# Optimization experiments

Hardware: AMD Instinct MI355X
Metric: run time of the kernel (lower is better)

The kernel has to match this reference:

```python
import jax, jax.numpy as jnp
import numpy as np

T, B, OBS, LS, H, NA = 256, 1024, 128, 128, 128, 18


def setup_inputs() -> dict:
    key = jax.random.key(0)
    ks = jax.random.split(key, 20)
    rn = lambda i, shape, sc: jax.random.normal(ks[i], shape, dtype=jnp.float32) * sc
    return {
        "x": jax.random.normal(ks[0], (T * B, OBS), dtype=jnp.float32),
        "done": (jax.random.uniform(ks[1], (T * B,)) < 0.05).astype(jnp.float32),
        "h0": rn(2, (1, B, H), 0.1),
        "c0": rn(3, (1, B, H), 0.1),
        # MLP encoder: obs -> 128 -> 32 -> lstm_size
        "W1": rn(4, (128, OBS), 0.1), "b1": jnp.zeros((128,), jnp.float32),
        "W2": rn(5, (32, 128), 0.1), "b2": jnp.zeros((32,), jnp.float32),
        "W3": rn(6, (LS, 32), 0.1), "b3": jnp.zeros((LS,), jnp.float32),
        # LSTM params, PyTorch gate order [i, f, g, o]
        "Wih": rn(7, (4 * H, LS), 0.1), "Whh": rn(8, (4 * H, H), 0.1),
        "bih": jnp.zeros((4 * H,), jnp.float32), "bhh": jnp.zeros((4 * H,), jnp.float32),
        "Wa": rn(9, (NA, H), 0.01), "ba": jnp.zeros((NA,), jnp.float32),
        "Wc": rn(10, (1, H), 0.1), "bc": jnp.zeros((1,), jnp.float32),
    }


def reference(x, done, h0, c0, W1, b1, W2, b2, W3, b3, Wih, Whh, bih, bhh, Wa, ba, Wc, bc):
    # MLP encoder (self.network)
    hid = jax.nn.relu(x @ W1.T + b1)
    hid = jax.nn.relu(hid @ W2.T + b2)
    hid = jax.nn.relu(hid @ W3.T + b3)           # [T*B, LS]
    Bsz = h0.shape[1]
    hid = hid.reshape(-1, Bsz, hid.shape[-1])    # [T, B, LS]
    d = done.reshape(-1, Bsz)                    # [T, B]

    Hh = h0.shape[-1]

    def step(carry, inp):
        h, c = carry
        xt, dt = inp
        m = (1.0 - dt)[:, None]                  # reset mask
        h = h * m
        c = c * m
        gates = xt @ Wih.T + bih + h @ Whh.T + bhh   # [B, 4H]
        i = jax.nn.sigmoid(gates[:, :Hh])
        f = jax.nn.sigmoid(gates[:, Hh:2 * Hh])
        g = jnp.tanh(gates[:, 2 * Hh:3 * Hh])
        o = jax.nn.sigmoid(gates[:, 3 * Hh:])
        c = f * c + i * g
        h = o * jnp.tanh(c)
        return (h, c), h

    (hN, cN), hs = jax.lax.scan(step, (h0[0], c0[0]), (hid, d))
    flat = hs.reshape(-1, Hh)                    # [T*B, H]
    logits = flat @ Wa.T + ba                    # actor head
    value = flat @ Wc.T + bc                     # critic head
    return jnp.concatenate([logits, value], axis=-1)  # [T*B, NA+1]
```

## Files before the change

kernel.cpp:

```cpp
#include <hip/hip_runtime.h>
#include <hip/hip_bf16.h>

typedef unsigned short u16;
typedef unsigned int u32;
typedef __attribute__((ext_vector_type(8))) short short8;
typedef __attribute__((ext_vector_type(4))) float f4;
typedef __attribute__((ext_vector_type(4))) u32 u4;

#define MFMA(a, b, c) __builtin_amdgcn_mfma_f32_16x16x32_bf16((a), (b), (c), 0, 0, 0)

#define TT 256
#define BB 1024
#define NN (TT * BB)
#define L2E 1.442695040888963f
#define WS_HID3 0
#define WS_WF   (NN * 128)
#define OFF_W1  0
#define OFF_W2  16384
#define OFF_W3  20480
#define OFF_WIH 24576
#define OFF_WHH 90112
#define OFF_WA  155648
#define WF_TOT  159744

static __device__ __forceinline__ u16 f2bf(float f) {
    u32 u = __float_as_uint(f);
    u32 r = (u + 0x7FFFu + ((u >> 16) & 1u)) >> 16;
    return (u16)r;
}
static __device__ __forceinline__ short8 pack8(f4 a, f4 b) {
    short8 r;
    r[0] = (short)f2bf(a[0]); r[1] = (short)f2bf(a[1]);
    r[2] = (short)f2bf(a[2]); r[3] = (short)f2bf(a[3]);
    r[4] = (short)f2bf(b[0]); r[5] = (short)f2bf(b[1]);
    r[6] = (short)f2bf(b[2]); r[7] = (short)f2bf(b[3]);
    return r;
}
static __device__ __forceinline__ short8 u4_to_s8(u4 v) {
    union { u4 u; short8 s; } t; t.u = v; return t.s;
}
static __device__ __forceinline__ float sig_pre(float x) {
    return __builtin_amdgcn_rcpf(1.f + __builtin_amdgcn_exp2f(-x));
}
static __device__ __forceinline__ float tanhf_fast(float x) {
    return 2.f * __builtin_amdgcn_rcpf(1.f + __builtin_amdgcn_exp2f(-2.885390081777927f * x)) - 1.f;
}

static __device__ void convW128(const float* src, int Nn, u16* dst, int tid, int nth) {
    int tot = Nn * 128;
    for (int d = tid; d < tot; d += nth) {
        int j = d & 7, l = (d >> 3) & 63, ck = d >> 9;
        int kc = ck & 3, nt = ck >> 2;
        int n = nt * 16 + (l & 15), k = kc * 32 + ((l >> 4) << 3) + j;
        dst[d] = f2bf(src[n * 128 + k]);
    }
}
static __device__ void convW128g(const float* src, u16* dst, int tid, int nth) {
    int tot = 512 * 128;
    for (int d = tid; d < tot; d += nth) {
        int j = d & 7, l = (d >> 3) & 63, ck = d >> 9;
        int kc = ck & 3, nt = ck >> 2;
        int n = nt * 16 + (l & 15), k = kc * 32 + ((l >> 4) << 3) + j;
        float sc = ((n >> 7) == 2) ? (2.f * L2E) : L2E;
        dst[d] = f2bf(src[n * 128 + k] * sc);
    }
}
static __device__ void convW32(const float* src, int Nn, u16* dst, int tid, int nth) {
    int tot = Nn * 32;
    for (int d = tid; d < tot; d += nth) {
        int j = d & 7, l = (d >> 3) & 63, nt = d >> 9;
        int n = nt * 16 + (l & 15), k = ((l >> 4) << 3) + j;
        dst[d] = f2bf(src[n * 32 + k]);
    }
}

__global__ void k0_conv(const float* __restrict__ W1, const float* __restrict__ W2,
                        const float* __restrict__ W3, const float* __restrict__ Wih,
                        const float* __restrict__ Whh, const float* __restrict__ Wa,
                        const float* __restrict__ Wc, u16* __restrict__ wf) {
    int tid = blockIdx.x * blockDim.x + threadIdx.x;
    int nth = gridDim.x * blockDim.x;
    convW128(W1, 128, wf + OFF_W1, tid, nth);
    convW128(W2, 32, wf + OFF_W2, tid, nth);
    convW32(W3, 128, wf + OFF_W3, tid, nth);
    convW128g(Wih, wf + OFF_WIH, tid, nth);
    convW128g(Whh, wf + OFF_WHH, tid, nth);
    for (int d = tid; d < 32 * 128; d += nth) {
        int j = d & 7, l = (d >> 3) & 63, ck = d >> 9;
        int kc = ck & 3, nt = ck >> 2;
        int n = nt * 16 + (l & 15), k = kc * 32 + ((l >> 4) << 3) + j;
        float v = (n < 18) ? Wa[n * 128 + k] : ((n == 18) ? Wc[k] : 0.f);
        wf[OFF_WA + d] = f2bf(v);
    }
}

__global__ __launch_bounds__(256, 2) void k1_enc(
    const float* __restrict__ x, const float* __restrict__ b1, const float* __restrict__ b2,
    const float* __restrict__ b3, const u16* __restrict__ wf, u16* __restrict__ hid3f) {
    __shared__ __align__(16) u16 scr[4][2560];

    int tid = threadIdx.x, wv = tid >> 6, lane = tid & 63;
    int m = lane & 15, q = lane >> 4;
    u16* s1 = scr[wv];
    u16* s2 = scr[wv] + 2048;
    const short8* W1v = (const short8*)(wf + OFF_W1);
    const short8* W2v = (const short8*)(wf + OFF_W2);
    const short8* W3v = (const short8*)(wf + OFF_W3);
    short8 w1r[32], w3r[8];
#pragma unroll
    for (int i = 0; i < 32; ++i) w1r[i] = W1v[i * 64 + lane];
#pragma unroll
    for (int i = 0; i < 8; ++i) w3r[i] = W3v[i * 64 + lane];
    int wid = blockIdx.x * 4 + wv;

    for (int it = 0; it < 8; ++it) {
        int c = wid + it * 2048;
        short8 a1[4];
        const float* xr = x + (size_t)(c * 16 + m) * 128 + q * 8;
#pragma unroll
        for (int kc = 0; kc < 4; ++kc) {
            f4 f0 = *(const f4*)(xr + kc * 32);
            f4 f1 = *(const f4*)(xr + kc * 32 + 4);
            a1[kc] = pack8(f0, f1);
        }
#pragma unroll
        for (int nt = 0; nt < 8; ++nt) {
            f4 acc = {0.f, 0.f, 0.f, 0.f};
#pragma unroll
            for (int kc = 0; kc < 4; ++kc) acc = MFMA(a1[kc], w1r[nt * 4 + kc], acc);
            int col = nt * 16 + m;
            float bb = b1[col];
            int base = (col >> 5) * 512 + ((col >> 3) & 3) * 128 + (col & 7);
#pragma unroll
            for (int p = 0; p < 4; ++p) {
                float v = acc[p] + bb; v = v > 0.f ? v : 0.f;
                s1[base + (q * 4 + p) * 8] = f2bf(v);
            }
        }
        asm volatile("s_waitcnt lgkmcnt(0)" ::: "memory");
        short8 a2[4];
#pragma unroll
        for (int kc = 0; kc < 4; ++kc) a2[kc] = *(const short8*)(s1 + kc * 512 + lane * 8);
#pragma unroll
        for (int nt = 0; nt < 2; ++nt) {
            f4 acc = {0.f, 0.f, 0.f, 0.f};
#pragma unroll
            for (int kc = 0; kc < 4; ++kc) acc = MFMA(a2[kc], W2v[(nt * 4 + kc) * 64 + lane], acc);
            int col = nt * 16 + m;
            float bb = b2[col];
            int base = (col >> 3) * 128 + (col & 7);
#pragma unroll
            for (int p = 0; p < 4; ++p) {
                float v = acc[p] + bb; v = v > 0.f ? v : 0.f;
                s2[base + (q * 4 + p) * 8] = f2bf(v);
            }
        }
        asm volatile("s_waitcnt lgkmcnt(0)" ::: "memory");
        short8 a3 = *(const short8*)(s2 + lane * 8);
#pragma unroll
        for (int nt = 0; nt < 8; ++nt) {
            f4 acc = {0.f, 0.f, 0.f, 0.f};
            acc = MFMA(a3, w3r[nt], acc);
            int col = nt * 16 + m;
            float bb = b3[col];
            int base = (col >> 5) * 512 + ((col >> 3) & 3) * 128 + (col & 7);
#pragma unroll
            for (int p = 0; p < 4; ++p) {
                float v = acc[p] + bb; v = v > 0.f ? v : 0.f;
                s1[base + (q * 4 + p) * 8] = f2bf(v);
            }
        }
        asm volatile("s_waitcnt lgkmcnt(0)" ::: "memory");
        int bI = c & 63, tt = c >> 6;
        u4* dst = (u4*)hid3f + ((size_t)bI * 256 + tt) * 256;
#pragma unroll
        for (int kc = 0; kc < 4; ++kc) dst[kc * 64 + lane] = *(const u4*)(s1 + kc * 512 + lane * 8);
    }
}

__global__ __launch_bounds__(512, 1) void k3_scan(
    const u16* __restrict__ hid3, const u16* __restrict__ wf,
    const float* __restrict__ bih, const float* __restrict__ bhh,
    const float* __restrict__ done, const float* __restrict__ h0, const float* __restrict__ c0,
    const float* __restrict__ ba, const float* __restrict__ bc, float* __restrict__ out) {
    __shared__ __align__(16) u16 hbuf[2][2048];
    __shared__ __align__(16) float dls[4096];

    int tid = threadIdx.x, wv = tid >> 6, lane = tid & 63;
    int m = lane & 15, q = lane >> 4;
    int bI = blockIdx.x, rb = bI * 16;
    int u = wv * 16 + m;

    const short8* WHv = (const short8*)(wf + OFF_WHH);
    const short8* WIv = (const short8*)(wf + OFF_WIH);
    const short8* WAv = (const short8*)(wf + OFF_WA);
    short8 wh[4][4], wi[4][4];
#pragma unroll
    for (int g = 0; g < 4; ++g)
#pragma unroll
        for (int kc = 0; kc < 4; ++kc) {
            int nt = g * 8 + wv;
            wh[g][kc] = WHv[(nt * 4 + kc) * 64 + lane];
            wi[g][kc] = WIv[(nt * 4 + kc) * 64 + lane];
        }
    float bg[4];
#pragma unroll
    for (int g = 0; g < 4; ++g) {
        float sc = (g == 2) ? (2.f * L2E) : L2E;
        bg[g] = (bih[g * 128 + u] + bhh[g * 128 + u]) * sc;
    }
    short8 wab[4];
    float hb = 0.f;
    int hcol = wv * 16 + m;
    if (wv < 2) {
#pragma unroll
        for (int kc = 0; kc < 4; ++kc) wab[kc] = WAv[(wv * 4 + kc) * 64 + lane];
        if (hcol < 18) hb = ba[hcol];
        else if (hcol == 18) hb = bc[0];
    }

    for (int i = tid; i < 4096; i += 512) {
        int t = i >> 4, r = i & 15;
        dls[i] = 1.0f - done[(size_t)t * BB + rb + r];
    }
    float cst[4];
#pragma unroll
    for (int k = 0; k < 4; ++k) {
        int r = 4 * q + k;
        cst[k] = c0[(size_t)(rb + r) * 128 + u];
        float hv = h0[(size_t)(rb + r) * 128 + u];
        hbuf[0][(u >> 5) * 512 + (((u >> 3) & 3) * 16 + r) * 8 + (u & 7)] = f2bf(hv);
    }
    const u4* h3 = (const u4*)hid3 + (size_t)bI * 65536;
    u4 xf[4];
#pragma unroll
    for (int kc = 0; kc < 4; ++kc) xf[kc] = h3[kc * 64 + lane];
    __syncthreads();

    for (int t = 0; t < TT; ++t) {
        const u16* hc = hbuf[t & 1];
        u16* hn = hbuf[(t + 1) & 1];
        short8 ah[4];
#pragma unroll
        for (int kc = 0; kc < 4; ++kc) ah[kc] = *(const short8*)(hc + kc * 512 + lane * 8);
        f4 aH[4], aX[4];
#pragma unroll
        for (int g = 0; g < 4; ++g) {
            aH[g] = (f4){0.f, 0.f, 0.f, 0.f};
            aX[g] = (f4){bg[g], bg[g], bg[g], bg[g]};
        }
#pragma unroll
        for (int kc = 0; kc < 4; ++kc) {
            short8 xs = u4_to_s8(xf[kc]);
#pragma unroll
            for (int g = 0; g < 4; ++g) {
                aH[g] = MFMA(ah[kc], wh[g][kc], aH[g]);
                aX[g] = MFMA(xs, wi[g][kc], aX[g]);
            }
        }
        if (t < TT - 1) {
#pragma unroll
            for (int kc = 0; kc < 4; ++kc)
                xf[kc] = h3[(size_t)(t + 1) * 256 + kc * 64 + lane];
        }
        if (wv < 2 && t > 0) {
            f4 hacc = {0.f, 0.f, 0.f, 0.f};
#pragma unroll
            for (int kc = 0; kc < 4; ++kc) hacc = MFMA(ah[kc], wab[kc], hacc);
            if (hcol < 19) {
                size_t n0 = (size_t)(t - 1) * 1024 + rb + 4 * q;
#pragma unroll
                for (int p = 0; p < 4; ++p) out[(n0 + p) * 19 + hcol] = hacc[p] + hb;
            }
        }
        f4 dm = *(const f4*)(dls + t * 16 + 4 * q);
#pragma unroll
        for (int k = 0; k < 4; ++k) {
            float mm = dm[k];
            float ip = aX[0][k] + mm * aH[0][k];
            float fp = aX[1][k] + mm * aH[1][k];
            float gp = aX[2][k] + mm * aH[2][k];
            float op = aX[3][k] + mm * aH[3][k];
            float ii = sig_pre(ip), ff = sig_pre(fp), oo = sig_pre(op);
            float gg = 2.f * sig_pre(gp) - 1.f;
            float cc = ff * (mm * cst[k]) + ii * gg;
            cst[k] = cc;
            float hh = oo * tanhf_fast(cc);
            hn[(u >> 5) * 512 + (((u >> 3) & 3) * 16 + (4 * q + k)) * 8 + (u & 7)] = f2bf(hh);
        }
        asm volatile("s_waitcnt lgkmcnt(0)" ::: "memory");
        __builtin_amdgcn_s_barrier();
        asm volatile("" ::: "memory");
    }
    if (wv < 2) {
        short8 ah[4];
#pragma unroll
        for (int kc = 0; kc < 4; ++kc) ah[kc] = *(const short8*)(hbuf[0] + kc * 512 + lane * 8);
        f4 hacc = {0.f, 0.f, 0.f, 0.f};
#pragma unroll
        for (int kc = 0; kc < 4; ++kc) hacc = MFMA(ah[kc], wab[kc], hacc);
        if (hcol < 19) {
            size_t n0 = (size_t)255 * 1024 + rb + 4 * q;
#pragma unroll
            for (int p = 0; p < 4; ++p) out[(n0 + p) * 19 + hcol] = hacc[p] + hb;
        }
    }
}

extern "C" void kernel_launch(void* const* d_in, const int* in_sizes, int n_in,
                              void* d_out, int out_size, void* d_ws, size_t ws_size,
                              hipStream_t stream) {
    const float* x    = (const float*)d_in[0];
    const float* done = (const float*)d_in[1];
    const float* h0   = (const float*)d_in[2];
    const float* c0   = (const float*)d_in[3];
    const float* W1   = (const float*)d_in[4];
    const float* b1   = (const float*)d_in[5];
    const float* W2   = (const float*)d_in[6];
    const float* b2   = (const float*)d_in[7];
    const float* W3   = (const float*)d_in[8];
    const float* b3   = (const float*)d_in[9];
    const float* Wih  = (const float*)d_in[10];
    const float* Whh  = (const float*)d_in[11];
    const float* bih  = (const float*)d_in[12];
    const float* bhh  = (const float*)d_in[13];
    const float* Wa   = (const float*)d_in[14];
    const float* ba   = (const float*)d_in[15];
    const float* Wc   = (const float*)d_in[16];
    const float* bc   = (const float*)d_in[17];
    float* out = (float*)d_out;

    u16* ws = (u16*)d_ws;
    u16* hid3f = ws + WS_HID3;
    u16* wf    = ws + WS_WF;

    hipLaunchKernelGGL(k0_conv, dim3(128), dim3(256), 0, stream,
                       W1, W2, W3, Wih, Whh, Wa, Wc, wf);
    hipLaunchKernelGGL(k1_enc, dim3(512), dim3(256), 0, stream,
                       x, b1, b2, b3, wf, hid3f);
    hipLaunchKernelGGL(k3_scan, dim3(64), dim3(512), 0, stream,
                       hid3f, wf, bih, bhh, done, h0, c0, ba, bc, out);
}
```

Measured before the change: 532.8 us.

## Double-buffer LSTM input prefetch two steps ahead and pin weight registers

Splits the per-step input fragment into two register buffers so the hid3 load for step t+2 is issued while step t runs, giving global loads a full extra timestep of latency hiding. The time loop is unrolled by two through an always-inline lambda. Empty asm constraints pin the weight fragments in VGPRs to discourage rematerialization or spilling. The input-projection MFMAs now run before the recurrent ones, and the done-mask LDS read is hoisted to the start of each step. The cost is extra register pressure from the second buffer, which may lower occupancy or cause spills.

```diff
diff --git a/kernel.cpp b/kernel.cpp
--- a/kernel.cpp
+++ b/kernel.cpp
@@ -22,6 +22,8 @@
 #define OFF_WHH 90112
 #define OFF_WA  155648
 #define WF_TOT  159744
+
+#define PIN4(a, b, c, d) asm volatile("" : "+v"(a), "+v"(b), "+v"(c), "+v"(d))
 
 static __device__ __forceinline__ u16 f2bf(float f) {
     u32 u = __float_as_uint(f);
@@ -232,14 +234,28 @@
         hbuf[0][(u >> 5) * 512 + (((u >> 3) & 3) * 16 + r) * 8 + (u & 7)] = f2bf(hv);
     }
     const u4* h3 = (const u4*)hid3 + (size_t)bI * 65536;
-    u4 xf[4];
-#pragma unroll
-    for (int kc = 0; kc < 4; ++kc) xf[kc] = h3[kc * 64 + lane];
+
+    u4 xfA[4], xfB[4];
+#pragma unroll
+    for (int kc = 0; kc < 4; ++kc) xfA[kc] = h3[kc * 64 + lane];
+#pragma unroll
+    for (int kc = 0; kc < 4; ++kc) xfB[kc] = h3[256 + kc * 64 + lane];
     __syncthreads();
 
-    for (int t = 0; t < TT; ++t) {
-        const u16* hc = hbuf[t & 1];
-        u16* hn = hbuf[(t + 1) & 1];
+    auto step = [&](int tc, u4 (&XU)[4]) __attribute__((always_inline)) {
+        PIN4(wh[0][0], wh[0][1], wh[0][2], wh[0][3]);
+        PIN4(wh[1][0], wh[1][1], wh[1][2], wh[1][3]);
+        PIN4(wh[2][0], wh[2][1], wh[2][2], wh[2][3]);
+        PIN4(wh[3][0], wh[3][1], wh[3][2], wh[3][3]);
+        PIN4(wi[0][0], wi[0][1], wi[0][2], wi[0][3]);
+        PIN4(wi[1][0], wi[1][1], wi[1][2], wi[1][3]);
+        PIN4(wi[2][0], wi[2][1], wi[2][2], wi[2][3]);
+        PIN4(wi[3][0], wi[3][1], wi[3][2], wi[3][3]);
+        PIN4(wab[0], wab[1], wab[2], wab[3]);
+
+        const u16* hc = hbuf[tc & 1];
+        u16* hn = hbuf[(tc + 1) & 1];
+        f4 dm = *(const f4*)(dls + tc * 16 + 4 * q);
         short8 ah[4];
 #pragma unroll
         for (int kc = 0; kc < 4; ++kc) ah[kc] = *(const short8*)(hc + kc * 512 + lane * 8);
@@ -251,29 +267,28 @@
         }
 #pragma unroll
         for (int kc = 0; kc < 4; ++kc) {
-            short8 xs = u4_to_s8(xf[kc]);
+            short8 xs = u4_to_s8(XU[kc]);
 #pragma unroll
             for (int g = 0; g < 4; ++g) {
+                aX[g] = MFMA(xs, wi[g][kc], aX[g]);
                 aH[g] = MFMA(ah[kc], wh[g][kc], aH[g]);
-                aX[g] = MFMA(xs, wi[g][kc], aX[g]);
-            }
-        }
-        if (t < TT - 1) {
+            }
+        }
+        if (tc + 2 < TT) {
 #pragma unroll
             for (int kc = 0; kc < 4; ++kc)
-                xf[kc] = h3[(size_t)(t + 1) * 256 + kc * 64 + lane];
-        }
-        if (wv < 2 && t > 0) {
+                XU[kc] = h3[(size_t)(tc + 2) * 256 + kc * 64 + lane];
+        }
+        if (wv < 2 && tc > 0) {
             f4 hacc = {0.f, 0.f, 0.f, 0.f};
 #pragma unroll
             for (int kc = 0; kc < 4; ++kc) hacc = MFMA(ah[kc], wab[kc], hacc);
             if (hcol < 19) {
-                size_t n0 = (size_t)(t - 1) * 1024 + rb + 4 * q;
+                size_t n0 = (size_t)(tc - 1) * 1024 + rb + 4 * q;
 #pragma unroll
                 for (int p = 0; p < 4; ++p) out[(n0 + p) * 19 + hcol] = hacc[p] + hb;
             }
         }
-        f4 dm = *(const f4*)(dls + t * 16 + 4 * q);
 #pragma unroll
         for (int k = 0; k < 4; ++k) {
             float mm = dm[k];
@@ -291,6 +306,11 @@
         asm volatile("s_waitcnt lgkmcnt(0)" ::: "memory");
         __builtin_amdgcn_s_barrier();
         asm volatile("" ::: "memory");
+    };
+
+    for (int t = 0; t < TT; t += 2) {
+        step(t, xfA);
+        step(t + 1, xfB);
     }
     if (wv < 2) {
         short8 ah[4];
```

Result: slower. 723.3 us (+35.8%).

## Precompute input gate projections in encoder and chunk scan into phases

Applied to the files above, without the earlier changes.

Moves the Wih·x input projection out of the serial LSTM scan into the parallel encoder kernel, which now writes fp16 gate pre-activations with the fused bias. The timeline is split into 8 phases of 32 steps, alternating encoder and scan launches and carrying h/c state through workspace. The aim is to halve the MFMA work on the sequential critical path and keep the gate buffer small enough to stay cache-resident. Whh moves from registers to LDS. The costs are 16 kernel launches, an fp16 rounding of the gate inputs, and LDS reads of the weights on every step.

```diff
diff --git a/kernel.cpp b/kernel.cpp
--- a/kernel.cpp
+++ b/kernel.cpp
@@ -6,22 +6,30 @@
 typedef __attribute__((ext_vector_type(8))) short short8;
 typedef __attribute__((ext_vector_type(4))) float f4;
 typedef __attribute__((ext_vector_type(4))) u32 u4;
+typedef __attribute__((ext_vector_type(4))) _Float16 h4;
 
 #define MFMA(a, b, c) __builtin_amdgcn_mfma_f32_16x16x32_bf16((a), (b), (c), 0, 0, 0)
 
 #define TT 256
 #define BB 1024
-#define NN (TT * BB)
+#define LPH 32
+#define NPH 8
+#define ROWS_PH (LPH * BB)
 #define L2E 1.442695040888963f
-#define WS_HID3 0
-#define WS_WF   (NN * 128)
+
+#define WS_GX   0
+#define GX_SZ   (ROWS_PH * 512)
+#define WS_WF   GX_SZ
 #define OFF_W1  0
 #define OFF_W2  16384
 #define OFF_W3  20480
 #define OFF_WIH 24576
 #define OFF_WHH 90112
 #define OFF_WA  155648
-#define WF_TOT  159744
+#define OFF_BGX 159744
+#define WF_TOT  160768
+#define WS_STH  (WS_WF + WF_TOT)
+#define WS_STC  (WS_STH + 131072)
 
 static __device__ __forceinline__ u16 f2bf(float f) {
     u32 u = __float_as_uint(f);
@@ -35,9 +43,6 @@
     r[4] = (short)f2bf(b[0]); r[5] = (short)f2bf(b[1]);
     r[6] = (short)f2bf(b[2]); r[7] = (short)f2bf(b[3]);
     return r;
-}
-static __device__ __forceinline__ short8 u4_to_s8(u4 v) {
-    union { u4 u; short8 s; } t; t.u = v; return t.s;
 }
 static __device__ __forceinline__ float sig_pre(float x) {
     return __builtin_amdgcn_rcpf(1.f + __builtin_amdgcn_exp2f(-x));
@@ -77,7 +82,8 @@
 __global__ void k0_conv(const float* __restrict__ W1, const float* __restrict__ W2,
                         const float* __restrict__ W3, const float* __restrict__ Wih,
                         const float* __restrict__ Whh, const float* __restrict__ Wa,
-                        const float* __restrict__ Wc, u16* __restrict__ wf) {
+                        const float* __restrict__ Wc, const float* __restrict__ bih,
+                        const float* __restrict__ bhh, u16* __restrict__ wf) {
     int tid = blockIdx.x * blockDim.x + threadIdx.x;
     int nth = gridDim.x * blockDim.x;
     convW128(W1, 128, wf + OFF_W1, tid, nth);
@@ -92,11 +98,16 @@
         float v = (n < 18) ? Wa[n * 128 + k] : ((n == 18) ? Wc[k] : 0.f);
         wf[OFF_WA + d] = f2bf(v);
     }
+    float* bgxf = (float*)(wf + OFF_BGX);
+    for (int d = tid; d < 512; d += nth) {
+        float sc = ((d >> 7) == 2) ? (2.f * L2E) : L2E;
+        bgxf[d] = (bih[d] + bhh[d]) * sc;
+    }
 }
 
 __global__ __launch_bounds__(256, 2) void k1_enc(
     const float* __restrict__ x, const float* __restrict__ b1, const float* __restrict__ b2,
-    const float* __restrict__ b3, const u16* __restrict__ wf, u16* __restrict__ hid3f) {
+    const float* __restrict__ b3, const u16* __restrict__ wf, u16* __restrict__ gx, int t0) {
     __shared__ __align__(16) u16 scr[4][2560];
 
     int tid = threadIdx.x, wv = tid >> 6, lane = tid & 63;
@@ -106,109 +117,106 @@
     const short8* W1v = (const short8*)(wf + OFF_W1);
     const short8* W2v = (const short8*)(wf + OFF_W2);
     const short8* W3v = (const short8*)(wf + OFF_W3);
-    short8 w1r[32], w3r[8];
-#pragma unroll
-    for (int i = 0; i < 32; ++i) w1r[i] = W1v[i * 64 + lane];
-#pragma unroll
-    for (int i = 0; i < 8; ++i) w3r[i] = W3v[i * 64 + lane];
+    const short8* WIv = (const short8*)(wf + OFF_WIH);
+    const float* bgxf = (const float*)(wf + OFF_BGX);
+
     int wid = blockIdx.x * 4 + wv;
-
-    for (int it = 0; it < 8; ++it) {
-        int c = wid + it * 2048;
-        short8 a1[4];
-        const float* xr = x + (size_t)(c * 16 + m) * 128 + q * 8;
-#pragma unroll
-        for (int kc = 0; kc < 4; ++kc) {
-            f4 f0 = *(const f4*)(xr + kc * 32);
-            f4 f1 = *(const f4*)(xr + kc * 32 + 4);
-            a1[kc] = pack8(f0, f1);
-        }
-#pragma unroll
-        for (int nt = 0; nt < 8; ++nt) {
-            f4 acc = {0.f, 0.f, 0.f, 0.f};
-#pragma unroll
-            for (int kc = 0; kc < 4; ++kc) acc = MFMA(a1[kc], w1r[nt * 4 + kc], acc);
-            int col = nt * 16 + m;
-            float bb = b1[col];
-            int base = (col >> 5) * 512 + ((col >> 3) & 3) * 128 + (col & 7);
-#pragma unroll
-            for (int p = 0; p < 4; ++p) {
-                float v = acc[p] + bb; v = v > 0.f ? v : 0.f;
-                s1[base + (q * 4 + p) * 8] = f2bf(v);
-            }
-        }
-        asm volatile("s_waitcnt lgkmcnt(0)" ::: "memory");
-        short8 a2[4];
-#pragma unroll
-        for (int kc = 0; kc < 4; ++kc) a2[kc] = *(const short8*)(s1 + kc * 512 + lane * 8);
-#pragma unroll
-        for (int nt = 0; nt < 2; ++nt) {
-            f4 acc = {0.f, 0.f, 0.f, 0.f};
-#pragma unroll
-            for (int kc = 0; kc < 4; ++kc) acc = MFMA(a2[kc], W2v[(nt * 4 + kc) * 64 + lane], acc);
-            int col = nt * 16 + m;
-            float bb = b2[col];
-            int base = (col >> 3) * 128 + (col & 7);
-#pragma unroll
-            for (int p = 0; p < 4; ++p) {
-                float v = acc[p] + bb; v = v > 0.f ? v : 0.f;
-                s2[base + (q * 4 + p) * 8] = f2bf(v);
-            }
-        }
-        asm volatile("s_waitcnt lgkmcnt(0)" ::: "memory");
-        short8 a3 = *(const short8*)(s2 + lane * 8);
-#pragma unroll
-        for (int nt = 0; nt < 8; ++nt) {
-            f4 acc = {0.f, 0.f, 0.f, 0.f};
-            acc = MFMA(a3, w3r[nt], acc);
-            int col = nt * 16 + m;
-            float bb = b3[col];
-            int base = (col >> 5) * 512 + ((col >> 3) & 3) * 128 + (col & 7);
-#pragma unroll
-            for (int p = 0; p < 4; ++p) {
-                float v = acc[p] + bb; v = v > 0.f ? v : 0.f;
-                s1[base + (q * 4 + p) * 8] = f2bf(v);
-            }
-        }
-        asm volatile("s_waitcnt lgkmcnt(0)" ::: "memory");
-        int bI = c & 63, tt = c >> 6;
-        u4* dst = (u4*)hid3f + ((size_t)bI * 256 + tt) * 256;
-#pragma unroll
-        for (int kc = 0; kc < 4; ++kc) dst[kc * 64 + lane] = *(const u4*)(s1 + kc * 512 + lane * 8);
+    int bI = wid & 63, tl = wid >> 6;
+
+    short8 a1[4];
+    const float* xr = x + ((size_t)(t0 + tl) * BB + bI * 16 + m) * 128 + q * 8;
+#pragma unroll
+    for (int kc = 0; kc < 4; ++kc) {
+        f4 f0 = *(const f4*)(xr + kc * 32);
+        f4 f1 = *(const f4*)(xr + kc * 32 + 4);
+        a1[kc] = pack8(f0, f1);
+    }
+#pragma unroll
+    for (int nt = 0; nt < 8; ++nt) {
+        f4 acc = {0.f, 0.f, 0.f, 0.f};
+#pragma unroll
+        for (int kc = 0; kc < 4; ++kc) acc = MFMA(a1[kc], W1v[(nt * 4 + kc) * 64 + lane], acc);
+        int col = nt * 16 + m;
+        float bb = b1[col];
+        int base = (col >> 5) * 512 + ((col >> 3) & 3) * 128 + (col & 7);
+#pragma unroll
+        for (int p = 0; p < 4; ++p) {
+            float v = acc[p] + bb; v = v > 0.f ? v : 0.f;
+            s1[base + (q * 4 + p) * 8] = f2bf(v);
+        }
+    }
+    asm volatile("s_waitcnt lgkmcnt(0)" ::: "memory");
+    short8 a2[4];
+#pragma unroll
+    for (int kc = 0; kc < 4; ++kc) a2[kc] = *(const short8*)(s1 + kc * 512 + lane * 8);
+#pragma unroll
+    for (int nt = 0; nt < 2; ++nt) {
+        f4 acc = {0.f, 0.f, 0.f, 0.f};
+#pragma unroll
+        for (int kc = 0; kc < 4; ++kc) acc = MFMA(a2[kc], W2v[(nt * 4 + kc) * 64 + lane], acc);
+        int col = nt * 16 + m;
+        float bb = b2[col];
+        int base = (col >> 3) * 128 + (col & 7);
+#pragma unroll
+        for (int p = 0; p < 4; ++p) {
+            float v = acc[p] + bb; v = v > 0.f ? v : 0.f;
+            s2[base + (q * 4 + p) * 8] = f2bf(v);
+        }
+    }
+    asm volatile("s_waitcnt lgkmcnt(0)" ::: "memory");
+    short8 a3 = *(const short8*)(s2 + lane * 8);
+#pragma unroll
+    for (int nt = 0; nt < 8; ++nt) {
+        f4 acc = {0.f, 0.f, 0.f, 0.f};
+        acc = MFMA(a3, W3v[nt * 64 + lane], acc);
+        int col = nt * 16 + m;
+        float bb = b3[col];
+        int base = (col >> 5) * 512 + ((col >> 3) & 3) * 128 + (col & 7);
+#pragma unroll
+        for (int p = 0; p < 4; ++p) {
+            float v = acc[p] + bb; v = v > 0.f ? v : 0.f;
+            s1[base + (q * 4 + p) * 8] = f2bf(v);
+        }
+    }
+    asm volatile("s_waitcnt lgkmcnt(0)" ::: "memory");
+    short8 a4[4];
+#pragma unroll
+    for (int kc = 0; kc < 4; ++kc) a4[kc] = *(const short8*)(s1 + kc * 512 + lane * 8);
+    _Float16* gxo = (_Float16*)gx + (size_t)(bI * LPH + tl) * 8192;
+#pragma unroll 4
+    for (int nt = 0; nt < 32; ++nt) {
+        f4 acc = {0.f, 0.f, 0.f, 0.f};
+#pragma unroll
+        for (int kc = 0; kc < 4; ++kc) acc = MFMA(a4[kc], WIv[(nt * 4 + kc) * 64 + lane], acc);
+        int col = nt * 16 + m;
+        float bb = bgxf[col];
+        h4 hv;
+#pragma unroll
+        for (int p = 0; p < 4; ++p) hv[p] = (_Float16)(acc[p] + bb);
+        *(h4*)(gxo + col * 16 + 4 * q) = hv;
     }
 }
 
 __global__ __launch_bounds__(512, 1) void k3_scan(
-    const u16* __restrict__ hid3, const u16* __restrict__ wf,
-    const float* __restrict__ bih, const float* __restrict__ bhh,
-    const float* __restrict__ done, const float* __restrict__ h0, const float* __restrict__ c0,
-    const float* __restrict__ ba, const float* __restrict__ bc, float* __restrict__ out) {
+    const u16* __restrict__ gx, const u16* __restrict__ wf, const float* __restrict__ done,
+    const float* __restrict__ h0, const float* __restrict__ c0,
+    u16* __restrict__ sth, float* __restrict__ stc,
+    const float* __restrict__ ba, const float* __restrict__ bc,
+    float* __restrict__ out, int t0) {
+    __shared__ __align__(16) u16 whl[65536];
     __shared__ __align__(16) u16 hbuf[2][2048];
-    __shared__ __align__(16) float dls[4096];
 
     int tid = threadIdx.x, wv = tid >> 6, lane = tid & 63;
     int m = lane & 15, q = lane >> 4;
     int bI = blockIdx.x, rb = bI * 16;
     int u = wv * 16 + m;
 
-    const short8* WHv = (const short8*)(wf + OFF_WHH);
-    const short8* WIv = (const short8*)(wf + OFF_WIH);
+    {
+        const u4* src = (const u4*)(wf + OFF_WHH);
+        u4* dst = (u4*)whl;
+        for (int i = tid; i < 8192; i += 512) dst[i] = src[i];
+    }
     const short8* WAv = (const short8*)(wf + OFF_WA);
-    short8 wh[4][4], wi[4][4];
-#pragma unroll
-    for (int g = 0; g < 4; ++g)
-#pragma unroll
-        for (int kc = 0; kc < 4; ++kc) {
-            int nt = g * 8 + wv;
-            wh[g][kc] = WHv[(nt * 4 + kc) * 64 + lane];
-            wi[g][kc] = WIv[(nt * 4 + kc) * 64 + lane];
-        }
-    float bg[4];
-#pragma unroll
-    for (int g = 0; g < 4; ++g) {
-        float sc = (g == 2) ? (2.f * L2E) : L2E;
-        bg[g] = (bih[g * 128 + u] + bhh[g * 128 + u]) * sc;
-    }
     short8 wab[4];
     float hb = 0.f;
     int hcol = wv * 16 + m;
@@ -218,81 +226,94 @@
         if (hcol < 18) hb = ba[hcol];
         else if (hcol == 18) hb = bc[0];
     }
-
-    for (int i = tid; i < 4096; i += 512) {
-        int t = i >> 4, r = i & 15;
-        dls[i] = 1.0f - done[(size_t)t * BB + rb + r];
-    }
     float cst[4];
 #pragma unroll
     for (int k = 0; k < 4; ++k) {
         int r = 4 * q + k;
-        cst[k] = c0[(size_t)(rb + r) * 128 + u];
-        float hv = h0[(size_t)(rb + r) * 128 + u];
-        hbuf[0][(u >> 5) * 512 + (((u >> 3) & 3) * 16 + r) * 8 + (u & 7)] = f2bf(hv);
-    }
-    const u4* h3 = (const u4*)hid3 + (size_t)bI * 65536;
-    u4 xf[4];
-#pragma unroll
-    for (int kc = 0; kc < 4; ++kc) xf[kc] = h3[kc * 64 + lane];
+        int hidx = (u >> 5) * 512 + (((u >> 3) & 3) * 16 + r) * 8 + (u & 7);
+        if (t0 == 0) {
+            cst[k] = c0[(size_t)(rb + r) * 128 + u];
+            hbuf[0][hidx] = f2bf(h0[(size_t)(rb + r) * 128 + u]);
+        } else {
+            cst[k] = stc[(size_t)(rb + r) * 128 + u];
+            hbuf[0][hidx] = sth[(size_t)(rb + r) * 128 + u];
+        }
+    }
+    const _Float16* gxf = (const _Float16*)gx + (size_t)bI * (LPH * 8192);
+    h4 gA[4], gB[4];
+    f4 dA, dB;
+#pragma unroll
+    for (int g = 0; g < 4; ++g) {
+        gA[g] = *(const h4*)(gxf + (g * 128 + u) * 16 + 4 * q);
+        gB[g] = *(const h4*)(gxf + 8192 + (g * 128 + u) * 16 + 4 * q);
+    }
+    dA = *(const f4*)(done + (size_t)t0 * BB + rb + 4 * q);
+    dB = *(const f4*)(done + (size_t)(t0 + 1) * BB + rb + 4 * q);
     __syncthreads();
 
-    for (int t = 0; t < TT; ++t) {
-        const u16* hc = hbuf[t & 1];
-        u16* hn = hbuf[(t + 1) & 1];
+    auto step = [&](int s, h4 (&GU)[4], f4& DU) __attribute__((always_inline)) {
+        const u16* hc = hbuf[s & 1];
+        u16* hn = hbuf[(s + 1) & 1];
         short8 ah[4];
 #pragma unroll
         for (int kc = 0; kc < 4; ++kc) ah[kc] = *(const short8*)(hc + kc * 512 + lane * 8);
-        f4 aH[4], aX[4];
-#pragma unroll
-        for (int g = 0; g < 4; ++g) {
-            aH[g] = (f4){0.f, 0.f, 0.f, 0.f};
-            aX[g] = (f4){bg[g], bg[g], bg[g], bg[g]};
-        }
-#pragma unroll
-        for (int kc = 0; kc < 4; ++kc) {
-            short8 xs = u4_to_s8(xf[kc]);
+        f4 aH[4];
+#pragma unroll
+        for (int g = 0; g < 4; ++g) aH[g] = (f4){0.f, 0.f, 0.f, 0.f};
+#pragma unroll
+        for (int kc = 0; kc < 4; ++kc)
 #pragma unroll
             for (int g = 0; g < 4; ++g) {
-                aH[g] = MFMA(ah[kc], wh[g][kc], aH[g]);
-                aX[g] = MFMA(xs, wi[g][kc], aX[g]);
+                short8 whf = *(const short8*)(whl + ((g * 8 + wv) * 4 + kc) * 512 + lane * 8);
+                aH[g] = MFMA(ah[kc], whf, aH[g]);
             }
-        }
-        if (t < TT - 1) {
-#pragma unroll
-            for (int kc = 0; kc < 4; ++kc)
-                xf[kc] = h3[(size_t)(t + 1) * 256 + kc * 64 + lane];
-        }
-        if (wv < 2 && t > 0) {
+        if (wv < 2 && (t0 + s) > 0) {
             f4 hacc = {0.f, 0.f, 0.f, 0.f};
 #pragma unroll
             for (int kc = 0; kc < 4; ++kc) hacc = MFMA(ah[kc], wab[kc], hacc);
             if (hcol < 19) {
-                size_t n0 = (size_t)(t - 1) * 1024 + rb + 4 * q;
+                size_t n0 = (size_t)(t0 + s - 1) * BB + rb + 4 * q;
 #pragma unroll
                 for (int p = 0; p < 4; ++p) out[(n0 + p) * 19 + hcol] = hacc[p] + hb;
             }
         }
-        f4 dm = *(const f4*)(dls + t * 16 + 4 * q);
+        f4 mmv, pre[4];
+#pragma unroll
+        for (int k = 0; k < 4; ++k) mmv[k] = 1.f - DU[k];
+#pragma unroll
+        for (int g = 0; g < 4; ++g)
+#pragma unroll
+            for (int k = 0; k < 4; ++k) pre[g][k] = (float)GU[g][k] + mmv[k] * aH[g][k];
+        if (s + 2 < LPH) {
+#pragma unroll
+            for (int g = 0; g < 4; ++g)
+                GU[g] = *(const h4*)(gxf + (size_t)(s + 2) * 8192 + (g * 128 + u) * 16 + 4 * q);
+            DU = *(const f4*)(done + (size_t)(t0 + s + 2) * BB + rb + 4 * q);
+        }
 #pragma unroll
         for (int k = 0; k < 4; ++k) {
-            float mm = dm[k];
-            float ip = aX[0][k] + mm * aH[0][k];
-            float fp = aX[1][k] + mm * aH[1][k];
-            float gp = aX[2][k] + mm * aH[2][k];
-            float op = aX[3][k] + mm * aH[3][k];
-            float ii = sig_pre(ip), ff = sig_pre(fp), oo = sig_pre(op);
-            float gg = 2.f * sig_pre(gp) - 1.f;
-            float cc = ff * (mm * cst[k]) + ii * gg;
+            float ii = sig_pre(pre[0][k]), ff = sig_pre(pre[1][k]), oo = sig_pre(pre[3][k]);
+            float gg = 2.f * sig_pre(pre[2][k]) - 1.f;
+            float cc = ff * (mmv[k] * cst[k]) + ii * gg;
             cst[k] = cc;
             float hh = oo * tanhf_fast(cc);
-            hn[(u >> 5) * 512 + (((u >> 3) & 3) * 16 + (4 * q + k)) * 8 + (u & 7)] = f2bf(hh);
+            u16 hbits = f2bf(hh);
+            hn[(u >> 5) * 512 + (((u >> 3) & 3) * 16 + (4 * q + k)) * 8 + (u & 7)] = hbits;
+            if (s == LPH - 1) {
+                sth[(size_t)(rb + 4 * q + k) * 128 + u] = hbits;
+                stc[(size_t)(rb + 4 * q + k) * 128 + u] = cc;
+            }
         }
         asm volatile("s_waitcnt lgkmcnt(0)" ::: "memory");
         __builtin_amdgcn_s_barrier();
         asm volatile("" ::: "memory");
-    }
-    if (wv < 2) {
+    };
+
+    for (int s = 0; s < LPH; s += 2) {
+        step(s, gA, dA);
+        step(s + 1, gB, dB);
+    }
+    if (t0 + LPH == TT && wv < 2) {
         short8 ah[4];
 #pragma unroll
         for (int kc = 0; kc < 4; ++kc) ah[kc] = *(const short8*)(hbuf[0] + kc * 512 + lane * 8);
@@ -300,7 +321,7 @@
 #pragma unroll
         for (int kc = 0; kc < 4; ++kc) hacc = MFMA(ah[kc], wab[kc], hacc);
         if (hcol < 19) {
-            size_t n0 = (size_t)255 * 1024 + rb + 4 * q;
+            size_t n0 = (size_t)(TT - 1) * BB + rb + 4 * q;
 #pragma unroll
             for (int p = 0; p < 4; ++p) out[(n0 + p) * 19 + hcol] = hacc[p] + hb;
         }
@@ -330,14 +351,19 @@
     const float* bc   = (const float*)d_in[17];
     float* out = (float*)d_out;
 
-    u16* ws = (u16*)d_ws;
-    u16* hid3f = ws + WS_HID3;
-    u16* wf    = ws + WS_WF;
+    u16* ws   = (u16*)d_ws;
+    u16* gxb  = ws + WS_GX;
+    u16* wf   = ws + WS_WF;
+    u16* sth  = ws + WS_STH;
+    float* stc = (float*)(ws + WS_STC);
 
     hipLaunchKernelGGL(k0_conv, dim3(128), dim3(256), 0, stream,
-                       W1, W2, W3, Wih, Whh, Wa, Wc, wf);
-    hipLaunchKernelGGL(k1_enc, dim3(512), dim3(256), 0, stream,
-                       x, b1, b2, b3, wf, hid3f);
-    hipLaunchKernelGGL(k3_scan, dim3(64), dim3(512), 0, stream,
-                       hid3f, wf, bih, bhh, done, h0, c0, ba, bc, out);
-}
+                       W1, W2, W3, Wih, Whh, Wa, Wc, bih, bhh, wf);
+    for (int ph = 0; ph < NPH; ++ph) {
+        int t0 = ph * LPH;
+        hipLaunchKernelGGL(k1_enc, dim3(512), dim3(256), 0, stream,
+                           x, b1, b2, b3, wf, gxb, t0);
+        hipLaunchKernelGGL(k3_scan, dim3(64), dim3(512), 0, stream,
+                           gxb, wf, done, h0, c0, sth, stc, ba, bc, out, t0);
+    }
+}
```

Measured after the change: 779.4 us. 46.3% more time.
